# Kernel optimization log

Hardware: AMD Instinct MI355X
Metric: run time of the kernel (lower is better)

## Reference

```python
import jax, jax.numpy as jnp
import numpy as np

N_FEAT = 7          # input_vector_size
M = 3               # memberships per feature (hardcoded 3 in torch module)
FUZZ = M ** N_FEAT  # 2187, cartesian product size
MID = 512
NUM_CLASS = 10
BATCH = 4096

# Precompute cartesian-product index table: itertools.product over rows of u[i]
# (last feature index varies fastest). IDX[k, i] = which of the 3 memberships of
# feature i appears in combination k.
_k = np.arange(FUZZ)
IDX = ((_k[:, None] // (M ** np.arange(N_FEAT - 1, -1, -1))[None, :]) % M).astype(np.int32)  # [FUZZ, N_FEAT]


def setup_inputs() -> dict:
    key = jax.random.key(0)
    ks = jax.random.split(key, 8)
    x = jax.random.normal(ks[0], (BATCH, N_FEAT), dtype=jnp.float32)
    # Parameters (xavier-ish init for weights, ones for b/bais as in torch init)
    c = jax.random.uniform(ks[1], (N_FEAT, M), minval=-1.0, maxval=1.0, dtype=jnp.float32)
    b = jnp.ones((N_FEAT, M), dtype=jnp.float32)
    wei = jax.random.uniform(ks[2], (FUZZ * N_FEAT, FUZZ), minval=-0.01, maxval=0.01, dtype=jnp.float32)
    bais = jnp.ones((1,), dtype=jnp.float32)
    W1 = jax.random.normal(ks[3], (MID, FUZZ), dtype=jnp.float32) * (1.0 / np.sqrt(FUZZ))
    b1 = jnp.zeros((MID,), dtype=jnp.float32)
    W2 = jax.random.normal(ks[4], (FUZZ, MID), dtype=jnp.float32) * (1.0 / np.sqrt(MID))
    b2 = jnp.zeros((FUZZ,), dtype=jnp.float32)
    W3 = jax.random.normal(ks[5], (NUM_CLASS, FUZZ), dtype=jnp.float32) * (1.0 / np.sqrt(FUZZ))
    b3 = jnp.zeros((NUM_CLASS,), dtype=jnp.float32)
    return {"x": x, "c": c, "b": b, "wei": wei, "bais": bais,
            "W1": W1, "b1": b1, "W2": W2, "b2": b2, "W3": W3, "b3": b3}


def reference(x, c, b, wei, bais, W1, b1, W2, b2, W3, b3):
    B = x.shape[0]
    # Gaussian fuzzy memberships: u[b, i, j] = exp(-(x[b,i]-c[i,j])^2 / b[i,j]^2)
    u = jnp.exp(-((x[:, :, None] - c[None]) ** 2) / (b[None] ** 2))  # [B, N_FEAT, M]
    # Cartesian product: dd[bt, k, i] = u[bt, i, IDX[k, i]]  (replaces itertools.product)
    idx = jnp.asarray(IDX)                       # [FUZZ, N_FEAT]
    feat = jnp.arange(N_FEAT)[None, :]           # [1, N_FEAT] broadcasts to [FUZZ, N_FEAT]
    dd = u[:, feat, idx]                         # [B, FUZZ, N_FEAT]
    # Fuzzy rule layer
    a = dd.reshape(B, FUZZ * N_FEAT) @ wei + bais            # [B, FUZZ]
    a_mean = a / jnp.sum(a, axis=1, keepdims=True)
    # Small residual MLP
    h1 = a_mean @ W1.T + b1                                   # [B, MID]
    h2 = h1 @ W2.T + b2                                       # [B, FUZZ]
    h3 = (a_mean + h2) @ W3.T + b3                            # [B, NUM_CLASS]
    out = jax.nn.leaky_relu(h3, negative_slope=0.2)
    # Dropout(0.5) omitted (eval mode / deterministic baseline)
    return out
```

## Files before the change

kernel.cpp:

```cpp
#include <hip/hip_runtime.h>

#define FUZZ 2187
#define NFEAT 7
#define MID 512
#define NCLS 10
#define BATCH 4096
#define SSTR 2192

__global__ __launch_bounds__(256) void k_reduce_wei(const float* __restrict__ wei,
                                                    float* __restrict__ S) {
    int n = blockIdx.x * 256 + threadIdx.x;
    if (n >= FUZZ) return;
    float acc[21];
#pragma unroll
    for (int t = 0; t < 21; ++t) acc[t] = 0.f;
    int k0 = blockIdx.y * 27;
    for (int kk = 0; kk < 27; ++kk) {
        int k = k0 + kk;
        int t = k;
        int d[7];
        d[6] = t % 3; t /= 3;
        d[5] = t % 3; t /= 3;
        d[4] = t % 3; t /= 3;
        d[3] = t % 3; t /= 3;
        d[2] = t % 3; t /= 3;
        d[1] = t % 3; t /= 3;
        d[0] = t;
        const float* rowp = wei + (size_t)(k * 7) * FUZZ + n;
#pragma unroll
        for (int j = 0; j < 7; ++j) {
            float v = rowp[(size_t)j * FUZZ];
            int m = d[j];
            acc[j * 3 + 0] += (m == 0) ? v : 0.f;
            acc[j * 3 + 1] += (m == 1) ? v : 0.f;
            acc[j * 3 + 2] += (m == 2) ? v : 0.f;
        }
    }
#pragma unroll
    for (int t = 0; t < 21; ++t)
        atomicAdd(&S[t * SSTR + n], acc[t]);
}

__device__ __forceinline__ float wave_sum(float v) {
#pragma unroll
    for (int off = 32; off > 0; off >>= 1) v += __shfl_down(v, off, 64);
    return v;
}

__global__ __launch_bounds__(64) void k_sw1(const float* __restrict__ S,
                                            const float* __restrict__ W1,
                                            float* __restrict__ SW1,
                                            float* __restrict__ ws1) {
    int i = blockIdx.x;
    int lane = threadIdx.x;
    float acc[21];
    float aw = 0.f;
#pragma unroll
    for (int t = 0; t < 21; ++t) acc[t] = 0.f;
    for (int n = lane; n < FUZZ; n += 64) {
        float w1 = W1[(size_t)i * FUZZ + n];
        aw += w1;
#pragma unroll
        for (int t = 0; t < 21; ++t) acc[t] += S[t * SSTR + n] * w1;
    }
#pragma unroll
    for (int t = 0; t < 21; ++t) acc[t] = wave_sum(acc[t]);
    aw = wave_sum(aw);
    if (lane == 0) {
#pragma unroll
        for (int t = 0; t < 21; ++t) SW1[t * MID + i] = acc[t];
        ws1[i] = aw;
    }
}

__global__ __launch_bounds__(64) void k_g(const float* __restrict__ SW1,
                                          const float* __restrict__ ws1,
                                          const float* __restrict__ b1,
                                          const float* __restrict__ W2,
                                          float* __restrict__ G,
                                          float* __restrict__ q,
                                          float* __restrict__ p) {
    int n = blockIdx.x;
    int lane = threadIdx.x;
    float acc[21];
    float aq = 0.f, ap = 0.f;
#pragma unroll
    for (int t = 0; t < 21; ++t) acc[t] = 0.f;
    for (int i = lane; i < MID; i += 64) {
        float w2 = W2[(size_t)n * MID + i];
        aq += ws1[i] * w2;
        ap += b1[i] * w2;
#pragma unroll
        for (int t = 0; t < 21; ++t) acc[t] += SW1[t * MID + i] * w2;
    }
#pragma unroll
    for (int t = 0; t < 21; ++t) acc[t] = wave_sum(acc[t]);
    aq = wave_sum(aq);
    ap = wave_sum(ap);
    if (lane == 0) {
#pragma unroll
        for (int t = 0; t < 21; ++t) G[t * SSTR + n] = acc[t];
        q[n] = aq;
        p[n] = ap;
    }
}

__global__ __launch_bounds__(64) void k_h(const float* __restrict__ S,
                                          const float* __restrict__ G,
                                          const float* __restrict__ q,
                                          const float* __restrict__ p,
                                          const float* __restrict__ b2,
                                          const float* __restrict__ b3,
                                          const float* __restrict__ W3,
                                          float* __restrict__ H,
                                          float* __restrict__ v,
                                          float* __restrict__ w,
                                          float* __restrict__ T) {
    int c = blockIdx.x;
    int lane = threadIdx.x;
    if (c < NCLS) {
        float acc[21];
        float av = 0.f, aw = 0.f;
#pragma unroll
        for (int t = 0; t < 21; ++t) acc[t] = 0.f;
        for (int n = lane; n < FUZZ; n += 64) {
            float w3 = W3[(size_t)c * FUZZ + n];
            av += (1.0f + q[n]) * w3;
            aw += (p[n] + b2[n]) * w3;
#pragma unroll
            for (int t = 0; t < 21; ++t)
                acc[t] += (S[t * SSTR + n] + G[t * SSTR + n]) * w3;
        }
#pragma unroll
        for (int t = 0; t < 21; ++t) acc[t] = wave_sum(acc[t]);
        av = wave_sum(av);
        aw = wave_sum(aw);
        if (lane == 0) {
#pragma unroll
            for (int t = 0; t < 21; ++t) H[t * NCLS + c] = acc[t];
            v[c] = av;
            w[c] = aw + b3[c];
        }
    } else {
        float acc[21];
#pragma unroll
        for (int t = 0; t < 21; ++t) acc[t] = 0.f;
        for (int n = lane; n < FUZZ; n += 64) {
#pragma unroll
            for (int t = 0; t < 21; ++t) acc[t] += S[t * SSTR + n];
        }
#pragma unroll
        for (int t = 0; t < 21; ++t) acc[t] = wave_sum(acc[t]);
        if (lane == 0) {
#pragma unroll
            for (int t = 0; t < 21; ++t) T[t] = acc[t];
        }
    }
}

__global__ __launch_bounds__(256) void k_out(const float* __restrict__ x,
                                             const float* __restrict__ cc,
                                             const float* __restrict__ bbv,
                                             const float* __restrict__ bais,
                                             const float* __restrict__ T,
                                             const float* __restrict__ H,
                                             const float* __restrict__ v,
                                             const float* __restrict__ w,
                                             float* __restrict__ out) {
    int b = blockIdx.x * 256 + threadIdx.x;
    if (b >= BATCH) return;
    float xv[NFEAT];
#pragma unroll
    for (int j = 0; j < NFEAT; ++j) xv[j] = x[b * NFEAT + j];
    float u[21];
#pragma unroll
    for (int j = 0; j < NFEAT; ++j) {
#pragma unroll
        for (int m = 0; m < 3; ++m) {
            float d = xv[j] - cc[j * 3 + m];
            float bv = bbv[j * 3 + m];
            u[j * 3 + m] = expf(-(d * d) / (bv * bv));
        }
    }
    float ba = bais[0];
    float r = 2187.0f * ba;
#pragma unroll
    for (int t = 0; t < 21; ++t) r += u[t] * T[t];
    float inv = 1.0f / r;
#pragma unroll
    for (int c = 0; c < NCLS; ++c) {
        float s = 0.f;
#pragma unroll
        for (int t = 0; t < 21; ++t) s += u[t] * H[t * NCLS + c];
        float h = (s + ba * v[c]) * inv + w[c];
        out[b * NCLS + c] = (h >= 0.f) ? h : 0.2f * h;
    }
}

extern "C" void kernel_launch(void* const* d_in, const int* in_sizes, int n_in,
                              void* d_out, int out_size, void* d_ws, size_t ws_size,
                              hipStream_t stream) {
    const float* x    = (const float*)d_in[0];
    const float* c    = (const float*)d_in[1];
    const float* bbv  = (const float*)d_in[2];
    const float* wei  = (const float*)d_in[3];
    const float* bais = (const float*)d_in[4];
    const float* W1   = (const float*)d_in[5];
    const float* b1   = (const float*)d_in[6];
    const float* W2   = (const float*)d_in[7];
    const float* b2   = (const float*)d_in[8];
    const float* W3   = (const float*)d_in[9];
    const float* b3   = (const float*)d_in[10];

    float* ws  = (float*)d_ws;
    float* S   = ws;
    float* G   = S + 21 * SSTR;
    float* SW1 = G + 21 * SSTR;
    float* ws1 = SW1 + 21 * MID;
    float* q   = ws1 + MID;
    float* p   = q + SSTR;
    float* T   = p + SSTR;
    float* H   = T + 32;
    float* v   = H + 224;
    float* w   = v + 16;

    hipMemsetAsync(S, 0, (size_t)(21 * SSTR) * sizeof(float), stream);
    k_reduce_wei<<<dim3(9, 81), 256, 0, stream>>>(wei, S);
    k_sw1<<<MID, 64, 0, stream>>>(S, W1, SW1, ws1);
    k_g<<<FUZZ, 64, 0, stream>>>(SW1, ws1, b1, W2, G, q, p);
    k_h<<<NCLS + 1, 64, 0, stream>>>(S, G, q, p, b2, b3, W3, H, v, w, T);
    k_out<<<(BATCH + 255) / 256, 256, 0, stream>>>(x, c, bbv, bais, T, H, v, w,
                                                   (float*)d_out);
}
```

Before: 304.5 us.

## Simplify wei reduction indexing and widen parallelism across downstream small kernels

Each y-block of the wei reduction now covers a fixed 27-rule chunk whose top four digits are constant, so four features accumulate into scalars and the last three use compile-time bins. This cuts the per-element select arithmetic and the atomics per thread from 21 to 13. k_sw1 and k_g use multi-wave blocks with a shared-memory reduction. k_h is split across 9 chunks with atomics, which needs an extra memset, and k_out uses 64-thread blocks to spread over more CUs. The extra atomics and memset add small overheads, and atomic accumulation order makes the float results slightly nondeterministic.

```diff
diff --git a/kernel.cpp b/kernel.cpp
--- a/kernel.cpp
+++ b/kernel.cpp
@@ -11,34 +11,35 @@
                                                     float* __restrict__ S) {
     int n = blockIdx.x * 256 + threadIdx.x;
     if (n >= FUZZ) return;
-    float acc[21];
-#pragma unroll
-    for (int t = 0; t < 21; ++t) acc[t] = 0.f;
-    int k0 = blockIdx.y * 27;
+    int by = blockIdx.y;
+    int t = by;
+    int d3 = t % 3; t /= 3;
+    int d2 = t % 3; t /= 3;
+    int d1 = t % 3; t /= 3;
+    int d0 = t;
+    float accL0 = 0.f, accL1 = 0.f, accL2 = 0.f, accL3 = 0.f;
+    float accH[9];
+#pragma unroll
+    for (int m = 0; m < 9; ++m) accH[m] = 0.f;
+    const float* base = wei + (size_t)(by * 189) * FUZZ + n;
+#pragma unroll
     for (int kk = 0; kk < 27; ++kk) {
-        int k = k0 + kk;
-        int t = k;
-        int d[7];
-        d[6] = t % 3; t /= 3;
-        d[5] = t % 3; t /= 3;
-        d[4] = t % 3; t /= 3;
-        d[3] = t % 3; t /= 3;
-        d[2] = t % 3; t /= 3;
-        d[1] = t % 3; t /= 3;
-        d[0] = t;
-        const float* rowp = wei + (size_t)(k * 7) * FUZZ + n;
-#pragma unroll
-        for (int j = 0; j < 7; ++j) {
-            float v = rowp[(size_t)j * FUZZ];
-            int m = d[j];
-            acc[j * 3 + 0] += (m == 0) ? v : 0.f;
-            acc[j * 3 + 1] += (m == 1) ? v : 0.f;
-            acc[j * 3 + 2] += (m == 2) ? v : 0.f;
-        }
-    }
-#pragma unroll
-    for (int t = 0; t < 21; ++t)
-        atomicAdd(&S[t * SSTR + n], acc[t]);
+        const float* rowp = base + (size_t)(kk * 7) * FUZZ;
+        accL0 += rowp[0];
+        accL1 += rowp[(size_t)1 * FUZZ];
+        accL2 += rowp[(size_t)2 * FUZZ];
+        accL3 += rowp[(size_t)3 * FUZZ];
+        accH[0 + kk / 9]       += rowp[(size_t)4 * FUZZ];
+        accH[3 + (kk / 3) % 3] += rowp[(size_t)5 * FUZZ];
+        accH[6 + kk % 3]       += rowp[(size_t)6 * FUZZ];
+    }
+    atomicAdd(&S[(0 + d0) * SSTR + n], accL0);
+    atomicAdd(&S[(3 + d1) * SSTR + n], accL1);
+    atomicAdd(&S[(6 + d2) * SSTR + n], accL2);
+    atomicAdd(&S[(9 + d3) * SSTR + n], accL3);
+#pragma unroll
+    for (int m = 0; m < 9; ++m)
+        atomicAdd(&S[(12 + m) * SSTR + n], accH[m]);
 }
 
 __device__ __forceinline__ float wave_sum(float v) {
@@ -47,18 +48,19 @@
     return v;
 }
 
-__global__ __launch_bounds__(64) void k_sw1(const float* __restrict__ S,
-                                            const float* __restrict__ W1,
-                                            float* __restrict__ SW1,
-                                            float* __restrict__ ws1) {
+__global__ __launch_bounds__(256) void k_sw1(const float* __restrict__ S,
+                                             const float* __restrict__ W1,
+                                             float* __restrict__ SW1,
+                                             float* __restrict__ ws1) {
     int i = blockIdx.x;
-    int lane = threadIdx.x;
+    int tid = threadIdx.x;
     float acc[21];
     float aw = 0.f;
 #pragma unroll
     for (int t = 0; t < 21; ++t) acc[t] = 0.f;
-    for (int n = lane; n < FUZZ; n += 64) {
-        float w1 = W1[(size_t)i * FUZZ + n];
+    const float* w1row = W1 + (size_t)i * FUZZ;
+    for (int n = tid; n < FUZZ; n += 256) {
+        float w1 = w1row[n];
         aw += w1;
 #pragma unroll
         for (int t = 0; t < 21; ++t) acc[t] += S[t * SSTR + n] * w1;
@@ -66,28 +68,37 @@
 #pragma unroll
     for (int t = 0; t < 21; ++t) acc[t] = wave_sum(acc[t]);
     aw = wave_sum(aw);
+    __shared__ float red[4][22];
+    int w = tid >> 6, lane = tid & 63;
     if (lane == 0) {
 #pragma unroll
-        for (int t = 0; t < 21; ++t) SW1[t * MID + i] = acc[t];
-        ws1[i] = aw;
-    }
-}
-
-__global__ __launch_bounds__(64) void k_g(const float* __restrict__ SW1,
-                                          const float* __restrict__ ws1,
-                                          const float* __restrict__ b1,
-                                          const float* __restrict__ W2,
-                                          float* __restrict__ G,
-                                          float* __restrict__ q,
-                                          float* __restrict__ p) {
+        for (int t = 0; t < 21; ++t) red[w][t] = acc[t];
+        red[w][21] = aw;
+    }
+    __syncthreads();
+    if (tid < 22) {
+        float s = red[0][tid] + red[1][tid] + red[2][tid] + red[3][tid];
+        if (tid < 21) SW1[tid * MID + i] = s;
+        else          ws1[i] = s;
+    }
+}
+
+__global__ __launch_bounds__(128) void k_g(const float* __restrict__ SW1,
+                                           const float* __restrict__ ws1,
+                                           const float* __restrict__ b1,
+                                           const float* __restrict__ W2,
+                                           float* __restrict__ G,
+                                           float* __restrict__ q,
+                                           float* __restrict__ p) {
     int n = blockIdx.x;
-    int lane = threadIdx.x;
+    int tid = threadIdx.x;
     float acc[21];
     float aq = 0.f, ap = 0.f;
 #pragma unroll
     for (int t = 0; t < 21; ++t) acc[t] = 0.f;
-    for (int i = lane; i < MID; i += 64) {
-        float w2 = W2[(size_t)n * MID + i];
+    const float* w2row = W2 + (size_t)n * MID;
+    for (int i = tid; i < MID; i += 128) {
+        float w2 = w2row[i];
         aq += ws1[i] * w2;
         ap += b1[i] * w2;
 #pragma unroll
@@ -97,11 +108,20 @@
     for (int t = 0; t < 21; ++t) acc[t] = wave_sum(acc[t]);
     aq = wave_sum(aq);
     ap = wave_sum(ap);
+    __shared__ float red[2][23];
+    int w = tid >> 6, lane = tid & 63;
     if (lane == 0) {
 #pragma unroll
-        for (int t = 0; t < 21; ++t) G[t * SSTR + n] = acc[t];
-        q[n] = aq;
-        p[n] = ap;
+        for (int t = 0; t < 21; ++t) red[w][t] = acc[t];
+        red[w][21] = aq;
+        red[w][22] = ap;
+    }
+    __syncthreads();
+    if (tid < 23) {
+        float s = red[0][tid] + red[1][tid];
+        if (tid < 21)      G[tid * SSTR + n] = s;
+        else if (tid == 21) q[n] = s;
+        else                p[n] = s;
     }
 }
 
@@ -117,13 +137,15 @@
                                           float* __restrict__ w,
                                           float* __restrict__ T) {
     int c = blockIdx.x;
+    int chunk = blockIdx.y;
     int lane = threadIdx.x;
+    int n0 = chunk * 243;
     if (c < NCLS) {
         float acc[21];
         float av = 0.f, aw = 0.f;
 #pragma unroll
         for (int t = 0; t < 21; ++t) acc[t] = 0.f;
-        for (int n = lane; n < FUZZ; n += 64) {
+        for (int n = n0 + lane; n < n0 + 243; n += 64) {
             float w3 = W3[(size_t)c * FUZZ + n];
             av += (1.0f + q[n]) * w3;
             aw += (p[n] + b2[n]) * w3;
@@ -137,15 +159,15 @@
         aw = wave_sum(aw);
         if (lane == 0) {
 #pragma unroll
-            for (int t = 0; t < 21; ++t) H[t * NCLS + c] = acc[t];
-            v[c] = av;
-            w[c] = aw + b3[c];
+            for (int t = 0; t < 21; ++t) atomicAdd(&H[t * NCLS + c], acc[t]);
+            atomicAdd(&v[c], av);
+            atomicAdd(&w[c], aw + (chunk == 0 ? b3[c] : 0.f));
         }
     } else {
         float acc[21];
 #pragma unroll
         for (int t = 0; t < 21; ++t) acc[t] = 0.f;
-        for (int n = lane; n < FUZZ; n += 64) {
+        for (int n = n0 + lane; n < n0 + 243; n += 64) {
 #pragma unroll
             for (int t = 0; t < 21; ++t) acc[t] += S[t * SSTR + n];
         }
@@ -153,21 +175,21 @@
         for (int t = 0; t < 21; ++t) acc[t] = wave_sum(acc[t]);
         if (lane == 0) {
 #pragma unroll
-            for (int t = 0; t < 21; ++t) T[t] = acc[t];
-        }
-    }
-}
-
-__global__ __launch_bounds__(256) void k_out(const float* __restrict__ x,
-                                             const float* __restrict__ cc,
-                                             const float* __restrict__ bbv,
-                                             const float* __restrict__ bais,
-                                             const float* __restrict__ T,
-                                             const float* __restrict__ H,
-                                             const float* __restrict__ v,
-                                             const float* __restrict__ w,
-                                             float* __restrict__ out) {
-    int b = blockIdx.x * 256 + threadIdx.x;
+            for (int t = 0; t < 21; ++t) atomicAdd(&T[t], acc[t]);
+        }
+    }
+}
+
+__global__ __launch_bounds__(64) void k_out(const float* __restrict__ x,
+                                            const float* __restrict__ cc,
+                                            const float* __restrict__ bbv,
+                                            const float* __restrict__ bais,
+                                            const float* __restrict__ T,
+                                            const float* __restrict__ H,
+                                            const float* __restrict__ v,
+                                            const float* __restrict__ w,
+                                            float* __restrict__ out) {
+    int b = blockIdx.x * 64 + threadIdx.x;
     if (b >= BATCH) return;
     float xv[NFEAT];
 #pragma unroll
@@ -225,10 +247,11 @@
     float* w   = v + 16;
 
     hipMemsetAsync(S, 0, (size_t)(21 * SSTR) * sizeof(float), stream);
+    hipMemsetAsync(T, 0, (size_t)288 * sizeof(float), stream);
     k_reduce_wei<<<dim3(9, 81), 256, 0, stream>>>(wei, S);
-    k_sw1<<<MID, 64, 0, stream>>>(S, W1, SW1, ws1);
-    k_g<<<FUZZ, 64, 0, stream>>>(SW1, ws1, b1, W2, G, q, p);
-    k_h<<<NCLS + 1, 64, 0, stream>>>(S, G, q, p, b2, b3, W3, H, v, w, T);
-    k_out<<<(BATCH + 255) / 256, 256, 0, stream>>>(x, c, bbv, bais, T, H, v, w,
-                                                   (float*)d_out);
-}
+    k_sw1<<<MID, 256, 0, stream>>>(S, W1, SW1, ws1);
+    k_g<<<FUZZ, 128, 0, stream>>>(SW1, ws1, b1, W2, G, q, p);
+    k_h<<<dim3(NCLS + 1, 9), 64, 0, stream>>>(S, G, q, p, b2, b3, W3, H, v, w, T);
+    k_out<<<(BATCH + 63) / 64, 64, 0, stream>>>(x, c, bbv, bais, T, H, v, w,
+                                                (float*)d_out);
+}
```

After: 319.9 us. 5.1% more time.
